# Kernel tuning notes

Hardware: AMD Instinct MI355X
Metric: run time of the kernel (lower is better)

## Reference

```python
import jax, jax.numpy as jnp
import numpy as np

POOLED_H = 7
POOLED_W = 7
SPATIAL_SCALE = 0.25
SAMPLING_RATIO = 2


def setup_inputs() -> dict:
    key = jax.random.key(0)
    k1, k2, k3, k4, k5, k6 = jax.random.split(key, 6)
    B, C, H, W = 2, 256, 200, 272
    N = 1000
    feat = jax.random.normal(k1, (B, C, H, W), dtype=jnp.float32)
    img_h = H / SPATIAL_SCALE  # 800
    img_w = W / SPATIAL_SCALE  # 1088
    bidx = jax.random.randint(k2, (N,), 0, B).astype(jnp.float32)
    x1 = jax.random.uniform(k3, (N,)) * (img_w - 64.0)
    y1 = jax.random.uniform(k4, (N,)) * (img_h - 64.0)
    bw = 16.0 + jax.random.uniform(k5, (N,)) * 200.0
    bh = 16.0 + jax.random.uniform(k6, (N,)) * 200.0
    rois = jnp.stack(
        [bidx, x1, y1, jnp.minimum(x1 + bw, img_w - 1.0), jnp.minimum(y1 + bh, img_h - 1.0)],
        axis=1,
    ).astype(jnp.float32)
    return {"feat": feat, "rois": rois}


def _roi_align(feat, rois):
    """Caffe2-style ROIAlign (aligned=False), avg pooling over sampling grid.
    feat: [B, C, H, W], rois: [N, 5] = [batch_ind, x1, y1, x2, y2] (image coords).
    Returns [N, C, POOLED_H, POOLED_W]."""
    B, C, H, W = feat.shape
    sr = SAMPLING_RATIO
    b = rois[:, 0].astype(jnp.int32)                      # [N]
    sw = rois[:, 1] * SPATIAL_SCALE
    sh = rois[:, 2] * SPATIAL_SCALE
    ew = rois[:, 3] * SPATIAL_SCALE
    eh = rois[:, 4] * SPATIAL_SCALE
    roi_w = jnp.maximum(ew - sw, 1.0)
    roi_h = jnp.maximum(eh - sh, 1.0)
    bin_w = roi_w / POOLED_W
    bin_h = roi_h / POOLED_H
    # Flattened sample coords: idx = ph*sr + i  ->  (idx+0.5)/sr = ph + (i+0.5)/sr
    oy = (jnp.arange(POOLED_H * sr, dtype=jnp.float32) + 0.5) / sr  # [Sy]
    ox = (jnp.arange(POOLED_W * sr, dtype=jnp.float32) + 0.5) / sr  # [Sx]
    ys = sh[:, None] + oy[None, :] * bin_h[:, None]                 # [N, Sy]
    xs = sw[:, None] + ox[None, :] * bin_w[:, None]                 # [N, Sx]
    # Out-of-image samples contribute 0 (CUDA kernel semantics: y < -1 or y > H)
    valid_y = (ys > -1.0) & (ys < H)
    valid_x = (xs > -1.0) & (xs < W)
    # Clamp + corner indices
    yc = jnp.clip(ys, 0.0, H - 1.0)
    xc = jnp.clip(xs, 0.0, W - 1.0)
    yl = jnp.floor(yc).astype(jnp.int32)
    xl = jnp.floor(xc).astype(jnp.int32)
    yh = jnp.minimum(yl + 1, H - 1)
    xh = jnp.minimum(xl + 1, W - 1)
    ly = yc - yl.astype(jnp.float32)   # [N, Sy]
    lx = xc - xl.astype(jnp.float32)   # [N, Sx]
    hy = 1.0 - ly
    hx = 1.0 - lx

    def gather(yi, xi):
        # [N, Sy, Sx, C]
        return feat[b[:, None, None], :, yi[:, :, None], xi[:, None, :]]

    val = (
        (hy[:, :, None] * hx[:, None, :])[..., None] * gather(yl, xl)
        + (hy[:, :, None] * lx[:, None, :])[..., None] * gather(yl, xh)
        + (ly[:, :, None] * hx[:, None, :])[..., None] * gather(yh, xl)
        + (ly[:, :, None] * lx[:, None, :])[..., None] * gather(yh, xh)
    )
    val = val * (valid_y[:, :, None] & valid_x[:, None, :])[..., None]
    N = rois.shape[0]
    # Average sr*sr samples per bin
    val = val.reshape(N, POOLED_H, sr, POOLED_W, sr, C).mean(axis=(2, 4))
    return val.transpose(0, 3, 1, 2)  # [N, C, PH, PW]


def reference(feat, rois):
    return _roi_align(feat, rois)
```

## Files before the change

### kernel.cpp

```cpp
#include <hip/hip_runtime.h>

#define PH 7
#define PW 7
#define SR 2
#define SY (PH * SR)
#define SX (PW * SR)
#define CH 256
#define FH 200
#define FW 272
#define BINS (PH * PW)
#define NPIX (FH * FW)

__device__ __forceinline__ unsigned short f2bf(float f) {
    unsigned x = __float_as_uint(f);
    return (unsigned short)((x + 0x7fffu + ((x >> 16) & 1u)) >> 16);
}
__device__ __forceinline__ float bflo(unsigned u) { return __uint_as_float(u << 16); }
__device__ __forceinline__ float bfhi(unsigned u) { return __uint_as_float(u & 0xffff0000u); }

__global__ __launch_bounds__(256) void transpose_kernel(
    const float* __restrict__ feat, unsigned short* __restrict__ featT) {
    __shared__ float tile[64][65];
    const int t  = threadIdx.x;
    const int w0 = blockIdx.x * 64;
    const int c0 = blockIdx.y * 64;
    const int bh = blockIdx.z;
    const int b  = bh / FH;
    const int h  = bh % FH;

    const int wq = t & 15;
    const int cl = t >> 4;
    if (w0 + wq * 4 < FW) {
        const size_t base = (size_t)b * CH * NPIX + (size_t)h * FW + w0 + wq * 4;
        #pragma unroll
        for (int k = 0; k < 4; ++k) {
            const int c = cl + 16 * k;
            const float4 v = *(const float4*)(feat + base + (size_t)(c0 + c) * NPIX);
            tile[wq * 4 + 0][c] = v.x;
            tile[wq * 4 + 1][c] = v.y;
            tile[wq * 4 + 2][c] = v.z;
            tile[wq * 4 + 3][c] = v.w;
        }
    }
    __syncthreads();

    const int cd = t & 31;
    const int wl = t >> 5;
    unsigned* __restrict__ dstu = (unsigned*)featT;
    #pragma unroll
    for (int k = 0; k < 8; ++k) {
        const int w = wl + 8 * k;
        if (w0 + w < FW) {
            const unsigned p = (unsigned)f2bf(tile[w][2 * cd])
                             | ((unsigned)f2bf(tile[w][2 * cd + 1]) << 16);
            const size_t pix = (size_t)bh * FW + w0 + w;
            dstu[pix * (CH / 2) + (c0 >> 1) + cd] = p;
        }
    }
}

__global__ __launch_bounds__(256) void roialign_cl_kernel(
    const unsigned short* __restrict__ featT,
    const float* __restrict__ rois,
    float* __restrict__ out, int N) {
    __shared__ int   s_yl[SY], s_yh[SY];
    __shared__ float s_ly[SY], s_hy[SY];
    __shared__ int   s_xl[SX], s_xh[SX];
    __shared__ float s_lx[SX], s_hx[SX];
    __shared__ unsigned short s_out16[CH * BINS];

    const int n   = blockIdx.x;
    const int tid = threadIdx.x;
    const float* __restrict__ roi = rois + (size_t)n * 5;

    if (tid < SY + SX) {
        const bool isy = (tid < SY);
        const int  idx = isy ? tid : tid - SY;
        const int  lim = isy ? FH : FW;
        const float start = (isy ? roi[2] : roi[1]) * 0.25f;
        const float end_  = (isy ? roi[4] : roi[3]) * 0.25f;
        const float len   = fmaxf(end_ - start, 1.0f);
        const float binsz = len * (isy ? (1.0f / PH) : (1.0f / PW));
        const float s = start + ((float)idx + 0.5f) * (1.0f / SR) * binsz;
        const float valid = (s > -1.0f && s < (float)lim) ? 1.0f : 0.0f;
        const float cc = fminf(fmaxf(s, 0.0f), (float)(lim - 1));
        const int   lo = (int)floorf(cc);
        const int   hi = min(lo + 1, lim - 1);
        const float l  = (cc - (float)lo) * valid;
        const float hw = (1.0f - (cc - (float)lo)) * valid;
        if (isy) { s_yl[idx] = lo * (FW * CH); s_yh[idx] = hi * (FW * CH);
                   s_ly[idx] = l; s_hy[idx] = hw; }
        else     { s_xl[idx] = lo * CH;        s_xh[idx] = hi * CH;
                   s_lx[idx] = l; s_hx[idx] = hw; }
    }
    __syncthreads();

    const int b    = (int)roi[0];
    const int m    = tid & 127;
    const int half = tid >> 7;
    const int c    = m * 2;
    const unsigned short* __restrict__ fbu =
        featT + (size_t)b * (FH * FW * CH) + c;

    const int bstart = half ? 25 : 0;
    const int bend   = half ? 49 : 25;

    #pragma unroll 1
    for (int bin = bstart; bin < bend; ++bin) {
        const int ph = bin / 7;
        const int pw = bin - ph * 7;
        const int sy = ph * SR, sx = pw * SR;
        float a0 = 0.0f, a1 = 0.0f;
        #pragma unroll
        for (int i = 0; i < SR; ++i) {
            const int   yo0 = s_yl[sy + i], yo1 = s_yh[sy + i];
            const float wy1 = s_ly[sy + i], wy0 = s_hy[sy + i];
            #pragma unroll
            for (int j = 0; j < SR; ++j) {
                const int   xo0 = s_xl[sx + j], xo1 = s_xh[sx + j];
                const float wx1 = s_lx[sx + j], wx0 = s_hx[sx + j];
                const unsigned u00 = *(const unsigned*)(fbu + yo0 + xo0);
                const unsigned u01 = *(const unsigned*)(fbu + yo0 + xo1);
                const unsigned u10 = *(const unsigned*)(fbu + yo1 + xo0);
                const unsigned u11 = *(const unsigned*)(fbu + yo1 + xo1);
                const float w00 = wy0 * wx0, w01 = wy0 * wx1;
                const float w10 = wy1 * wx0, w11 = wy1 * wx1;
                a0 += w00 * bflo(u00) + w01 * bflo(u01) + w10 * bflo(u10) + w11 * bflo(u11);
                a1 += w00 * bfhi(u00) + w01 * bfhi(u01) + w10 * bfhi(u10) + w11 * bfhi(u11);
            }
        }
        s_out16[c * BINS + bin]       = f2bf(a0 * 0.25f);
        s_out16[(c + 1) * BINS + bin] = f2bf(a1 * 0.25f);
    }
    __syncthreads();

    float* __restrict__ outn = out + (size_t)n * (CH * BINS);
    #pragma unroll
    for (int k = 0; k < BINS; ++k) {
        const int e = k * 256 + tid;
        outn[e] = bflo((unsigned)s_out16[e]);
    }
}

__global__ __launch_bounds__(256) void roialign_kernel(
    const float* __restrict__ feat,
    const float* __restrict__ rois,
    float* __restrict__ out, int N) {
    __shared__ int   s_yl[SY], s_yh[SY];
    __shared__ float s_ly[SY], s_hy[SY];
    __shared__ int   s_xl[SX], s_xh[SX];
    __shared__ float s_lx[SX], s_hx[SX];
    __shared__ float s_out[CH * BINS];

    const int n   = blockIdx.x;
    const int tid = threadIdx.x;
    const float* __restrict__ roi = rois + (size_t)n * 5;

    if (tid < SY + SX) {
        const bool isy = (tid < SY);
        const int  idx = isy ? tid : tid - SY;
        const int  lim = isy ? FH : FW;
        const float start = (isy ? roi[2] : roi[1]) * 0.25f;
        const float end_  = (isy ? roi[4] : roi[3]) * 0.25f;
        const float len   = fmaxf(end_ - start, 1.0f);
        const float binsz = len * (isy ? (1.0f / PH) : (1.0f / PW));
        const float s = start + ((float)idx + 0.5f) * (1.0f / SR) * binsz;
        const float valid = (s > -1.0f && s < (float)lim) ? 1.0f : 0.0f;
        const float cc = fminf(fmaxf(s, 0.0f), (float)(lim - 1));
        const int   lo = (int)floorf(cc);
        const int   hi = min(lo + 1, lim - 1);
        const float l  = (cc - (float)lo) * valid;
        const float hw = (1.0f - (cc - (float)lo)) * valid;
        if (isy) { s_yl[idx] = lo; s_yh[idx] = hi; s_ly[idx] = l; s_hy[idx] = hw; }
        else     { s_xl[idx] = lo; s_xh[idx] = hi; s_lx[idx] = l; s_hx[idx] = hw; }
    }
    __syncthreads();

    const int b = (int)roi[0];
    const int c = tid;
    const float* __restrict__ fp = feat + ((size_t)b * CH + c) * (size_t)NPIX;

    #pragma unroll 1
    for (int ph = 0; ph < PH; ++ph) {
        const int sy0 = ph * SR;
        const float* r00 = fp + s_yl[sy0] * FW;
        const float* r01 = fp + s_yh[sy0] * FW;
        const float* r10 = fp + s_yl[sy0 + 1] * FW;
        const float* r11 = fp + s_yh[sy0 + 1] * FW;
        const float ly0 = s_ly[sy0],     hy0 = s_hy[sy0];
        const float ly1 = s_ly[sy0 + 1], hy1 = s_hy[sy0 + 1];
        for (int pw = 0; pw < PW; ++pw) {
            const int sx0 = pw * SR;
            float acc = 0.0f;
            #pragma unroll
            for (int j = 0; j < SR; ++j) {
                const int   xl = s_xl[sx0 + j], xh = s_xh[sx0 + j];
                const float lx = s_lx[sx0 + j], hx = s_hx[sx0 + j];
                acc += hy0 * (hx * r00[xl] + lx * r00[xh])
                     + ly0 * (hx * r01[xl] + lx * r01[xh]);
                acc += hy1 * (hx * r10[xl] + lx * r10[xh])
                     + ly1 * (hx * r11[xl] + lx * r11[xh]);
            }
            s_out[c * BINS + ph * PW + pw] = acc * 0.25f;
        }
    }
    __syncthreads();

    float* __restrict__ outn = out + (size_t)n * (CH * BINS);
    #pragma unroll
    for (int k = 0; k < BINS; ++k) {
        const int idx = k * 256 + tid;
        outn[idx] = s_out[idx];
    }
}

extern "C" void kernel_launch(void* const* d_in, const int* in_sizes, int n_in,
                              void* d_out, int out_size, void* d_ws, size_t ws_size,
                              hipStream_t stream) {
    const float* feat = (const float*)d_in[0];
    const float* rois = (const float*)d_in[1];
    float* out = (float*)d_out;
    const int N = in_sizes[1] / 5;
    const int B = in_sizes[0] / (CH * NPIX);
    const size_t need = (size_t)B * CH * NPIX * sizeof(unsigned short);

    if (ws_size >= need) {
        unsigned short* featT = (unsigned short*)d_ws;
        dim3 tgrid((FW + 63) / 64, CH / 64, B * FH);
        transpose_kernel<<<tgrid, 256, 0, stream>>>(feat, featT);
        roialign_cl_kernel<<<N, 256, 0, stream>>>(featT, rois, out, N);
    } else {
        roialign_kernel<<<N, 256, 0, stream>>>(feat, rois, out, N);
    }
}
```

Before: 229.4 us.

## Restructure transpose to full-row tiles and widen ROIAlign loads to four channels

The transpose kernel now gives each block a whole feature row (all 272 columns) for 64 channels. It converts to bf16 before staging into shared memory and writes packed pairs straight from that tile, which drops the bounds checks and the odd grid. The ROIAlign kernel has each thread load uint2 (4 bf16 channels) per corner, split into four bin groups across 64-thread quarters. The 0.5 validity weight per axis absorbs the 1/4 averaging. The bf16 tile has no padding, so the strided column writes in the transpose may hit shared-memory bank conflicts.

```diff
diff --git a/kernel.cpp b/kernel.cpp
--- a/kernel.cpp
+++ b/kernel.cpp
@@ -20,42 +20,38 @@
 
 __global__ __launch_bounds__(256) void transpose_kernel(
     const float* __restrict__ feat, unsigned short* __restrict__ featT) {
-    __shared__ float tile[64][65];
+    __shared__ unsigned short tile[FW][64];
     const int t  = threadIdx.x;
-    const int w0 = blockIdx.x * 64;
+    const int bh = blockIdx.x;
     const int c0 = blockIdx.y * 64;
-    const int bh = blockIdx.z;
     const int b  = bh / FH;
     const int h  = bh % FH;
 
-    const int wq = t & 15;
-    const int cl = t >> 4;
-    if (w0 + wq * 4 < FW) {
-        const size_t base = (size_t)b * CH * NPIX + (size_t)h * FW + w0 + wq * 4;
-        #pragma unroll
-        for (int k = 0; k < 4; ++k) {
-            const int c = cl + 16 * k;
-            const float4 v = *(const float4*)(feat + base + (size_t)(c0 + c) * NPIX);
-            tile[wq * 4 + 0][c] = v.x;
-            tile[wq * 4 + 1][c] = v.y;
-            tile[wq * 4 + 2][c] = v.z;
-            tile[wq * 4 + 3][c] = v.w;
-        }
+    const int cl  = t >> 2;
+    const int wq0 = t & 3;
+    const float* __restrict__ src =
+        feat + (size_t)b * CH * NPIX + (size_t)(c0 + cl) * NPIX + (size_t)h * FW;
+    #pragma unroll
+    for (int k = 0; k < 17; ++k) {
+        const int fidx = wq0 + 4 * k;
+        const float4 v = *(const float4*)(src + fidx * 4);
+        const int w = fidx * 4;
+        tile[w + 0][cl] = f2bf(v.x);
+        tile[w + 1][cl] = f2bf(v.y);
+        tile[w + 2][cl] = f2bf(v.z);
+        tile[w + 3][cl] = f2bf(v.w);
     }
     __syncthreads();
 
     const int cd = t & 31;
     const int wl = t >> 5;
     unsigned* __restrict__ dstu = (unsigned*)featT;
-    #pragma unroll
-    for (int k = 0; k < 8; ++k) {
+    const size_t pixbase = (size_t)bh * FW;
+    #pragma unroll
+    for (int k = 0; k < 34; ++k) {
         const int w = wl + 8 * k;
-        if (w0 + w < FW) {
-            const unsigned p = (unsigned)f2bf(tile[w][2 * cd])
-                             | ((unsigned)f2bf(tile[w][2 * cd + 1]) << 16);
-            const size_t pix = (size_t)bh * FW + w0 + w;
-            dstu[pix * (CH / 2) + (c0 >> 1) + cd] = p;
-        }
+        const unsigned p = *(const unsigned*)&tile[w][2 * cd];
+        dstu[(pixbase + w) * (CH / 2) + (c0 >> 1) + cd] = p;
     }
 }
 
@@ -82,35 +78,35 @@
         const float len   = fmaxf(end_ - start, 1.0f);
         const float binsz = len * (isy ? (1.0f / PH) : (1.0f / PW));
         const float s = start + ((float)idx + 0.5f) * (1.0f / SR) * binsz;
-        const float valid = (s > -1.0f && s < (float)lim) ? 1.0f : 0.0f;
+        const float valid = (s > -1.0f && s < (float)lim) ? 0.5f : 0.0f;
         const float cc = fminf(fmaxf(s, 0.0f), (float)(lim - 1));
         const int   lo = (int)floorf(cc);
         const int   hi = min(lo + 1, lim - 1);
         const float l  = (cc - (float)lo) * valid;
         const float hw = (1.0f - (cc - (float)lo)) * valid;
-        if (isy) { s_yl[idx] = lo * (FW * CH); s_yh[idx] = hi * (FW * CH);
+        const int   rowstride = FW * (CH / 2);
+        if (isy) { s_yl[idx] = lo * rowstride; s_yh[idx] = hi * rowstride;
                    s_ly[idx] = l; s_hy[idx] = hw; }
-        else     { s_xl[idx] = lo * CH;        s_xh[idx] = hi * CH;
+        else     { s_xl[idx] = lo * (CH / 2);  s_xh[idx] = hi * (CH / 2);
                    s_lx[idx] = l; s_hx[idx] = hw; }
     }
     __syncthreads();
 
-    const int b    = (int)roi[0];
-    const int m    = tid & 127;
-    const int half = tid >> 7;
-    const int c    = m * 2;
-    const unsigned short* __restrict__ fbu =
-        featT + (size_t)b * (FH * FW * CH) + c;
-
-    const int bstart = half ? 25 : 0;
-    const int bend   = half ? 49 : 25;
+    const int b = (int)roi[0];
+    const int q = tid & 63;
+    const int g = tid >> 6;
+    const unsigned* __restrict__ fbu =
+        (const unsigned*)featT + (size_t)b * (FH * FW * (CH / 2)) + q * 2;
+
+    const int bstart = g * 12;
+    const int bend   = (g == 3) ? 49 : (g + 1) * 12;
 
     #pragma unroll 1
     for (int bin = bstart; bin < bend; ++bin) {
         const int ph = bin / 7;
         const int pw = bin - ph * 7;
         const int sy = ph * SR, sx = pw * SR;
-        float a0 = 0.0f, a1 = 0.0f;
+        float a0 = 0.f, a1 = 0.f, a2 = 0.f, a3 = 0.f;
         #pragma unroll
         for (int i = 0; i < SR; ++i) {
             const int   yo0 = s_yl[sy + i], yo1 = s_yh[sy + i];
@@ -119,18 +115,23 @@
             for (int j = 0; j < SR; ++j) {
                 const int   xo0 = s_xl[sx + j], xo1 = s_xh[sx + j];
                 const float wx1 = s_lx[sx + j], wx0 = s_hx[sx + j];
-                const unsigned u00 = *(const unsigned*)(fbu + yo0 + xo0);
-                const unsigned u01 = *(const unsigned*)(fbu + yo0 + xo1);
-                const unsigned u10 = *(const unsigned*)(fbu + yo1 + xo0);
-                const unsigned u11 = *(const unsigned*)(fbu + yo1 + xo1);
+                const uint2 u00 = *(const uint2*)(fbu + yo0 + xo0);
+                const uint2 u01 = *(const uint2*)(fbu + yo0 + xo1);
+                const uint2 u10 = *(const uint2*)(fbu + yo1 + xo0);
+                const uint2 u11 = *(const uint2*)(fbu + yo1 + xo1);
                 const float w00 = wy0 * wx0, w01 = wy0 * wx1;
                 const float w10 = wy1 * wx0, w11 = wy1 * wx1;
-                a0 += w00 * bflo(u00) + w01 * bflo(u01) + w10 * bflo(u10) + w11 * bflo(u11);
-                a1 += w00 * bfhi(u00) + w01 * bfhi(u01) + w10 * bfhi(u10) + w11 * bfhi(u11);
+                a0 += w00 * bflo(u00.x) + w01 * bflo(u01.x) + w10 * bflo(u10.x) + w11 * bflo(u11.x);
+                a1 += w00 * bfhi(u00.x) + w01 * bfhi(u01.x) + w10 * bfhi(u10.x) + w11 * bfhi(u11.x);
+                a2 += w00 * bflo(u00.y) + w01 * bflo(u01.y) + w10 * bflo(u10.y) + w11 * bflo(u11.y);
+                a3 += w00 * bfhi(u00.y) + w01 * bfhi(u01.y) + w10 * bfhi(u10.y) + w11 * bfhi(u11.y);
             }
         }
-        s_out16[c * BINS + bin]       = f2bf(a0 * 0.25f);
-        s_out16[(c + 1) * BINS + bin] = f2bf(a1 * 0.25f);
+        const int c4 = q * 4;
+        s_out16[(c4 + 0) * BINS + bin] = f2bf(a0);
+        s_out16[(c4 + 1) * BINS + bin] = f2bf(a1);
+        s_out16[(c4 + 2) * BINS + bin] = f2bf(a2);
+        s_out16[(c4 + 3) * BINS + bin] = f2bf(a3);
     }
     __syncthreads();
 
@@ -226,7 +227,7 @@
 
     if (ws_size >= need) {
         unsigned short* featT = (unsigned short*)d_ws;
-        dim3 tgrid((FW + 63) / 64, CH / 64, B * FH);
+        dim3 tgrid(B * FH, CH / 64);
         transpose_kernel<<<tgrid, 256, 0, stream>>>(feat, featT);
         roialign_cl_kernel<<<N, 256, 0, stream>>>(featT, rois, out, N);
     } else {
```

After: 223.9 us. 2.4% less time.
